# Performance work log

Measured on AMD Instinct MI355X. Metric: run time of the kernel, lower is better.

## Reference

```python
import jax, jax.numpy as jnp
import numpy as np

CHUNK = 32
EPS = 1e-6

def _l2norm(x):
    return x * jax.lax.rsqrt(jnp.sum(x * x, axis=-1, keepdims=True) + EPS)

def setup_inputs() -> dict:
    key = jax.random.key(0)
    k1, k2, k3, k4 = jax.random.split(key, 4)
    b, h, L, dk, dv = 4, 8, 4096, 128, 128
    return {
        'q': jax.random.normal(k1, (b, h, L, dk), dtype=jnp.float32),
        'k': jax.random.normal(k2, (b, h, L, dk), dtype=jnp.float32),
        'v': jax.random.normal(k3, (b, h, L, dv), dtype=jnp.float32),
        'beta': jax.random.uniform(k4, (b, h, L), dtype=jnp.float32),
    }

def _delta_rule_chunkwise(q, k, v, beta):
    b, h, L, dk = q.shape
    dv = v.shape[-1]
    c = CHUNK
    assert L % c == 0, 'L must be a multiple of chunk_size (no padding path)'
    n = L // c

    q = _l2norm(q)
    k = _l2norm(k)
    v = v * beta[..., None]
    k_beta = k * beta[..., None]

    # [b,h,n,c,d]
    resh = lambda t: t.reshape(b, h, n, c, t.shape[-1])
    qc, kc, vc, kbc = resh(q), resh(k), resh(v), resh(k_beta)

    ones = jnp.ones((c, c), dtype=jnp.float32)
    strict_lower = jnp.tril(ones, -1)      # below diagonal
    lower_inc = jnp.tril(ones, 0)          # diagonal and below

    # inv = -(k_beta @ k^T) with upper-incl-diag zeroed, then forward substitution
    inv = -jnp.einsum('bhncd,bhned->bhnce', kbc, kc) * strict_lower
    for i in range(1, c):
        # inv[..., i, :i] += inv[..., i, :] @ inv[..., :, :i]
        upd = jnp.einsum('bhnk,bhnkj->bhnj', inv[..., i, :], inv[..., :, :i])
        inv = inv.at[..., i, :i].add(upd)
    inv = inv + jnp.eye(c, dtype=inv.dtype)

    u = jnp.einsum('bhnce,bhned->bhncd', inv, vc)    # [b,h,n,c,dv]
    w = jnp.einsum('bhnce,bhned->bhncd', inv, kbc)   # [b,h,n,c,dk]

    # scan over chunks carrying state S [b,h,dk,dv]
    def step(S, inp):
        q_i, k_i, u0_i, w_i = inp  # [b,h,c,d*]
        attn = jnp.einsum('bhcd,bhed->bhce', q_i, k_i) * lower_inc
        u_i = u0_i - jnp.einsum('bhcd,bhdv->bhcv', w_i, S)
        out_i = jnp.einsum('bhcd,bhdv->bhcv', q_i, S) + jnp.einsum('bhce,bhev->bhcv', attn, u_i)
        S = S + jnp.einsum('bhcd,bhcv->bhdv', k_i, u_i)
        return S, out_i

    chunk_first = lambda t: jnp.moveaxis(t, 2, 0)  # [n,b,h,c,d]
    S0 = jnp.zeros((b, h, dk, dv), dtype=q.dtype)
    S, out = jax.lax.scan(step, S0, (chunk_first(qc), chunk_first(kc), chunk_first(u), chunk_first(w)))
    out = jnp.moveaxis(out, 0, 2).reshape(b, h, L, dv)
    return out, S

def reference(q, k, v, beta):
    out, S = _delta_rule_chunkwise(q, k, v, beta)
    return out
```

## Files before the change

### kernel.cpp

```cpp
#include <hip/hip_runtime.h>
#include <math.h>

#define CHUNK 32
#define DK 128
#define DV 128
#define L_SEQ 4096
#define BH 32
#define NCH 128

typedef __attribute__((ext_vector_type(8))) short bf16x8;
typedef __attribute__((ext_vector_type(4))) float f32x4;

union U8 { unsigned int u[4]; bf16x8 v; };

#define MFMA16(a, b, c) __builtin_amdgcn_mfma_f32_16x16x32_bf16((a), (b), (c), 0, 0, 0)
#define LGKM_WAIT() __asm__ __volatile__("s_waitcnt lgkmcnt(0)" ::: "memory")

__device__ __forceinline__ unsigned short f2bf(float x){
    unsigned int u = __builtin_bit_cast(unsigned int, x);
    u = u + 0x7FFFu + ((u >> 16) & 1u);
    return (unsigned short)(u >> 16);
}
__device__ __forceinline__ unsigned int pk2(float a, float b){
    unsigned int r;
    asm("v_cvt_pk_bf16_f32 %0, %1, %2" : "=v"(r) : "v"(a), "v"(b));
    return r;
}

__device__ __forceinline__ bf16x8 afragF32(const float (*M)[36], int row, int q8){
    float4 f0 = *(const float4*)&M[row][q8];
    float4 f1 = *(const float4*)&M[row][q8 + 4];
    U8 t;
    t.u[0] = pk2(f0.x, f0.y); t.u[1] = pk2(f0.z, f0.w);
    t.u[2] = pk2(f1.x, f1.y); t.u[3] = pk2(f1.z, f1.w);
    return t.v;
}
__device__ __forceinline__ bf16x8 bfragF32(const float (*M)[36], int q8, int col){
    U8 t;
#pragma unroll
    for (int j2 = 0; j2 < 4; ++j2)
        t.u[j2] = pk2(M[q8 + 2*j2][col], M[q8 + 2*j2 + 1][col]);
    return t.v;
}


template<bool WKT>
__global__ __launch_bounds__(64)
void prep_kernel(const float* __restrict__ q, const float* __restrict__ k,
                 const float* __restrict__ beta,
                 unsigned short* __restrict__ qw, unsigned short* __restrict__ kw,
                 unsigned short* __restrict__ Tw, unsigned short* __restrict__ Aw,
                 unsigned short* __restrict__ kwT)
{
    const int bc = blockIdx.x;
    const size_t row0 = (size_t)bc * CHUNK;
    const int l = threadIdx.x;
    const int quad = (l >> 4) & 3, ln15 = l & 15, q8 = quad * 8;

    __shared__ float Ms[32][36];
    __shared__ float Rs[32][36];
    __shared__ unsigned short knS[WKT ? 4392 : 2];

    const float bet0 = beta[row0 + ln15];
    const float bet1 = beta[row0 + 16 + ln15];

    bf16x8 qF[2][4];
    {
        float4 raw[2][4][2];
        float s0 = 0.f, s1 = 0.f;
#pragma unroll
        for (int mt = 0; mt < 2; ++mt)
#pragma unroll
        for (int ks = 0; ks < 4; ++ks){
            const float* p = q + (row0 + 16*mt + ln15) * DK + 32*ks + q8;
            raw[mt][ks][0] = *(const float4*)p;
            raw[mt][ks][1] = *(const float4*)(p + 4);
        }
#pragma unroll
        for (int ks = 0; ks < 4; ++ks)
#pragma unroll
        for (int h = 0; h < 2; ++h){
            float4 a = raw[0][ks][h], b = raw[1][ks][h];
            s0 += a.x*a.x + a.y*a.y + a.z*a.z + a.w*a.w;
            s1 += b.x*b.x + b.y*b.y + b.z*b.z + b.w*b.w;
        }
        s0 += __shfl_xor(s0, 16); s0 += __shfl_xor(s0, 32);
        s1 += __shfl_xor(s1, 16); s1 += __shfl_xor(s1, 32);
        float sc0 = rsqrtf(s0 + 1e-6f), sc1 = rsqrtf(s1 + 1e-6f);
#pragma unroll
        for (int mt = 0; mt < 2; ++mt){
            float sc = mt ? sc1 : sc0;
#pragma unroll
            for (int ks = 0; ks < 4; ++ks){
                float4 a = raw[mt][ks][0], b = raw[mt][ks][1];
// ... 16 lines not shown
            const float* p = k + (row0 + 16*mt + ln15) * DK + 32*ks + q8;
            raw[mt][ks][0] = *(const float4*)p;
            raw[mt][ks][1] = *(const float4*)(p + 4);
        }
#pragma unroll
        for (int ks = 0; ks < 4; ++ks)
#pragma unroll
        for (int h = 0; h < 2; ++h){
            float4 a = raw[0][ks][h], b = raw[1][ks][h];
            s0 += a.x*a.x + a.y*a.y + a.z*a.z + a.w*a.w;
            s1 += b.x*b.x + b.y*b.y + b.z*b.z + b.w*b.w;
        }
        s0 += __shfl_xor(s0, 16); s0 += __shfl_xor(s0, 32);
        s1 += __shfl_xor(s1, 16); s1 += __shfl_xor(s1, 32);
        float sc0 = rsqrtf(s0 + 1e-6f), sc1 = rsqrtf(s1 + 1e-6f);
#pragma unroll
        for (int mt = 0; mt < 2; ++mt){
            float sc = mt ? sc1 : sc0;
            float bb = mt ? bet1 : bet0;
#pragma unroll
            for (int ks = 0; ks < 4; ++ks){
                float4 a = raw[mt][ks][0], b = raw[mt][ks][1];
                float x0=a.x*sc, x1=a.y*sc, x2=a.z*sc, x3=a.w*sc;
                float x4=b.x*sc, x5=b.y*sc, x6=b.z*sc, x7=b.w*sc;
                U8 t, tb;
                t.u[0]=pk2(x0,x1); t.u[1]=pk2(x2,x3); t.u[2]=pk2(x4,x5); t.u[3]=pk2(x6,x7);
                tb.u[0]=pk2(x0*bb,x1*bb); tb.u[1]=pk2(x2*bb,x3*bb);
                tb.u[2]=pk2(x4*bb,x5*bb); tb.u[3]=pk2(x6*bb,x7*bb);
                kF[mt][ks] = t.v; kB[mt][ks] = tb.v;
                *(bf16x8*)(kw + (row0 + 16*mt + ln15) * DK + 32*ks + q8) = t.v;
            }
        }
    }

    if constexpr (WKT){
#pragma unroll
        for (int mt = 0; mt < 2; ++mt)
#pragma unroll
        for (int ks = 0; ks < 4; ++ks){
            int i = 16*mt + ln15;
            int ad = i * 136 + (i >> 3) * 16 + 32*ks + q8;
            *(bf16x8*)&knS[ad] = kF[mt][ks];
        }
    }

    f32x4 Z = {0.f, 0.f, 0.f, 0.f};
    f32x4 Bacc[2][2] = {{Z, Z}, {Z, Z}};
    f32x4 Aacc[2][2] = {{Z, Z}, {Z, Z}};
#pragma unroll
    for (int ks = 0; ks < 4; ++ks)
#pragma unroll
    for (int mt = 0; mt < 2; ++mt)
#pragma unroll
    for (int nt = 0; nt < 2; ++nt){
        Bacc[mt][nt] = MFMA16(kB[mt][ks], kF[nt][ks], Bacc[mt][nt]);
        Aacc[mt][nt] = MFMA16(qF[mt][ks], kF[nt][ks], Aacc[mt][nt]);
    }

    f32x4 Rc[2][2];
#pragma unroll
    for (int mt = 0; mt < 2; ++mt)
#pragma unroll
    for (int nt = 0; nt < 2; ++nt)
#pragma unroll
    for (int rg = 0; rg < 4; ++rg){
        int row = 16*mt + 4*quad + rg, col = 16*nt + ln15;
        float av = (col <= row) ? Aacc[mt][nt][rg] : 0.f;
        Aw[((size_t)bc << 10) + row*32 + col] = f2bf(av);
        float bm = (col < row) ? -Bacc[mt][nt][rg] : 0.f;
        Ms[row][col] = bm;
        Rc[mt][nt][rg] = bm + ((col == row) ? 1.f : 0.f);
    }

    if constexpr (WKT){
        unsigned short* kT = kwT + ((size_t)bc << 12);
#pragma unroll
        for (int t = 0; t < 8; ++t){
            unsigned short rj[8];
#pragma unroll
            for (int j = 0; j < 8; ++j)
                rj[j] = knS[(q8 + j) * 136 + ((q8 + j) >> 3) * 16 + 16*t + ln15];
            U8 kk;
            kk.u[0] = (unsigned)rj[0] | ((unsigned)rj[1] << 16);
            kk.u[1] = (unsigned)rj[2] | ((unsigned)rj[3] << 16);
            kk.u[2] = (unsigned)rj[4] | ((unsigned)rj[5] << 16);
            kk.u[3] = (unsigned)rj[6] | ((unsigned)rj[7] << 16);
            *(bf16x8*)(kT + (16*t + ln15) * 32 + q8) = kk.v;
        }
    }

#pragma unroll 1
    for (int rd = 0; rd < 4; ++rd){
        LGKM_WAIT();
        bf16x8 Am[2], Bm2[2];
#pragma unroll
        for (int mt = 0; mt < 2; ++mt) Am[mt] = afragF32(Ms, 16*mt + ln15, q8);
#pragma unroll
        for (int nt = 0; nt < 2; ++nt) Bm2[nt] = bfragF32(Ms, q8, 16*nt + ln15);
        f32x4 Mq[2][2];
#pragma unroll
        for (int mt = 0; mt < 2; ++mt)
#pragma unroll
        for (int nt = 0; nt < 2; ++nt)
            Mq[mt][nt] = MFMA16(Am[mt], Bm2[nt], Z);
#pragma unroll
        for (int mt = 0; mt < 2; ++mt)
#pragma unroll
        for (int nt = 0; nt < 2; ++nt)
#pragma unroll
        for (int rg = 0; rg < 4; ++rg){
            int row = 16*mt + 4*quad + rg, col = 16*nt + ln15;
            Rs[row][col] = Rc[mt][nt][rg];
            Ms[row][col] = Mq[mt][nt][rg];
        }
        LGKM_WAIT();
        bf16x8 Ar[2], Bq[2];
#pragma unroll
        for (int mt = 0; mt < 2; ++mt) Ar[mt] = afragF32(Rs, 16*mt + ln15, q8);
#pragma unroll
        for (int nt = 0; nt < 2; ++nt) Bq[nt] = bfragF32(Ms, q8, 16*nt + ln15);
#pragma unroll
        for (int mt = 0; mt < 2; ++mt)
#pragma unroll
        for (int nt = 0; nt < 2; ++nt)
            Rc[mt][nt] = MFMA16(Ar[mt], Bq[nt], Rc[mt][nt]);
    }

#pragma unroll
    for (int mt = 0; mt < 2; ++mt)
#pragma unroll
    for (int nt = 0; nt < 2; ++nt)
#pragma unroll
    for (int rg = 0; rg < 4; ++rg){
        int row = 16*mt + 4*quad + rg, col = 16*nt + ln15;
        Tw[((size_t)bc << 10) + row*32 + col] = f2bf(Rc[mt][nt][rg]);
    }
}


__global__ __launch_bounds__(64, 1)
void scan_fast(const float* __restrict__ v, const float* __restrict__ beta,
               const unsigned short* __restrict__ qw, const unsigned short* __restrict__ kw,
               const unsigned short* __restrict__ kwT,
               const unsigned short* __restrict__ Tw, const unsigned short* __restrict__ Aw,
               float* __restrict__ out)
{
    const int id = blockIdx.x;
    const int bh = id & 31, cb = id >> 5, c0 = cb * 16;
    const int l = threadIdx.x;
    const int quad = (l >> 4) & 3, ln15 = l & 15, q8 = quad * 8;
    const int hi = l >> 5;

    const f32x4 Z = {0.f, 0.f, 0.f, 0.f};
    f32x4 Sacc[8];
#pragma unroll
    for (int t = 0; t < 8; ++t) Sacc[t] = Z;

    const size_t bhL = (size_t)bh * L_SEQ;
    const int a0 = (((l & 16) << 1) | ln15) << 2;
    const int a1 = a0 + 64;

    bf16x8 cur[2][4], qA[2][4], knA[8], tA[2], aA[2], uB;
    float vr[8], br[8];

    auto quadswap = [&](int p0, int p1, int p2, int p3) -> bf16x8 {
        U8 r; int e, f;
        e = __builtin_amdgcn_ds_bpermute(a0, p0); f = __builtin_amdgcn_ds_bpermute(a0, p2);
        r.u[0] = (unsigned)(hi ? f : e);
        e = __builtin_amdgcn_ds_bpermute(a0, p1); f = __builtin_amdgcn_ds_bpermute(a0, p3);
        r.u[1] = (unsigned)(hi ? f : e);
        e = __builtin_amdgcn_ds_bpermute(a1, p0); f = __builtin_amdgcn_ds_bpermute(a1, p2);
// ... 32 lines not shown
            aA[mt] = *(const bf16x8*)(Ap + (16*mt + ln15) * 32 + q8);
    };
    auto loadVB = [&](int ch){
        const size_t row0 = bhL + (size_t)ch * CHUNK;
#pragma unroll
        for (int g = 0; g < 8; ++g){
            int i = 16*(g >> 2) + 4*quad + (g & 3);
            vr[g] = v[(row0 + i) * DV + c0 + ln15];
            br[g] = beta[row0 + i];
        }
    };
    auto loadKT = [&](int ch){
        const unsigned short* p = kwT + ((size_t)(bh * NCH + ch) << 12);
#pragma unroll
        for (int t = 0; t < 8; ++t)
            knA[t] = *(const bf16x8*)(p + (16*t + ln15) * 32 + q8);
    };

    loadK(0); loadQ(0); loadT(0); loadA(0); loadVB(0);
    {
        U8 z; z.u[0] = 0u; z.u[1] = 0u; z.u[2] = 0u; z.u[3] = 0u;
        uB = z.v;
#pragma unroll
        for (int t = 0; t < 8; ++t) knA[t] = z.v;
    }

    for (int ch = 0; ch < NCH; ++ch){
        const size_t row0 = bhL + (size_t)ch * CHUNK;
        const int chn = (ch + 1 < NCH) ? ch + 1 : NCH - 1;

#pragma unroll
        for (int t = 0; t < 8; ++t)
            Sacc[t] = MFMA16(knA[t], uB, Sacc[t]);

        loadKT(ch);

        int P[8][2];
#pragma unroll
        for (int t = 0; t < 8; ++t){
            P[t][0] = (int)pk2(Sacc[t][0], Sacc[t][1]);
            P[t][1] = (int)pk2(Sacc[t][2], Sacc[t][3]);
        }
        bf16x8 SB[4];
#pragma unroll
        for (int ks = 0; ks < 4; ++ks)
            SB[ks] = quadswap(P[2*ks][0], P[2*ks][1], P[2*ks+1][0], P[2*ks+1][1]);

        f32x4 Y[2] = {Z, Z}, Op[2] = {Z, Z};
#pragma unroll
        for (int ks = 0; ks < 4; ++ks)
#pragma unroll
        for (int mt = 0; mt < 2; ++mt){
            Y[mt]  = MFMA16(cur[mt][ks], SB[ks], Y[mt]);
            Op[mt] = MFMA16(qA[mt][ks],  SB[ks], Op[mt]);
        }

        loadK(chn); loadQ(chn);

        int PX0, PX1, PX2, PX3;
        {
            float x00 = br[0]*(vr[0]-Y[0][0]), x01 = br[1]*(vr[1]-Y[0][1]);
            float x02 = br[2]*(vr[2]-Y[0][2]), x03 = br[3]*(vr[3]-Y[0][3]);
            float x10 = br[4]*(vr[4]-Y[1][0]), x11 = br[5]*(vr[5]-Y[1][1]);
            float x12 = br[6]*(vr[6]-Y[1][2]), x13 = br[7]*(vr[7]-Y[1][3]);
            PX0 = (int)pk2(x00, x01); PX1 = (int)pk2(x02, x03);
            PX2 = (int)pk2(x10, x11); PX3 = (int)pk2(x12, x13);
        }
        bf16x8 Xb = quadswap(PX0, PX1, PX2, PX3);

        f32x4 U[2];
#pragma unroll
        for (int mt = 0; mt < 2; ++mt) U[mt] = MFMA16(tA[mt], Xb, Z);

        loadT(chn);

        {
            int PU0 = (int)pk2(U[0][0], U[0][1]), PU1 = (int)pk2(U[0][2], U[0][3]);
            int PU2 = (int)pk2(U[1][0], U[1][1]), PU3 = (int)pk2(U[1][2], U[1][3]);
            uB = quadswap(PU0, PU1, PU2, PU3);
        }

        f32x4 O[2];
#pragma unroll
        for (int mt = 0; mt < 2; ++mt) O[mt] = MFMA16(aA[mt], uB, Op[mt]);
#pragma unroll
        for (int mt = 0; mt < 2; ++mt)
#pragma unroll
        for (int rg = 0; rg < 4; ++rg)
            out[(row0 + 16*mt + 4*quad + rg) * DV + c0 + ln15] = O[mt][rg];

        loadA(chn);
        loadVB(chn);
    }
}


__global__ __launch_bounds__(64, 1)
void scan_kernel(const float* __restrict__ v, const float* __restrict__ beta,
                 const unsigned short* __restrict__ qw, const unsigned short* __restrict__ kw,
                 const unsigned short* __restrict__ Tw, const unsigned short* __restrict__ Aw,
                 float* __restrict__ out)
{
    const int id = blockIdx.x;
    const int bh = id & 31, cb = id >> 5, c0 = cb * 16;
    const int l = threadIdx.x;
    const int quad = (l >> 4) & 3, ln15 = l & 15, q8 = quad * 8;
    const int hi = l >> 5;

    __shared__ unsigned short knR[4392];
    __shared__ unsigned short Xt[16][40];
    __shared__ unsigned short ut[16][40];

    const f32x4 Z = {0.f, 0.f, 0.f, 0.f};
    f32x4 Sacc[8];
#pragma unroll
    for (int t = 0; t < 8; ++t) Sacc[t] = Z;

    const size_t bhL = (size_t)bh * L_SEQ;
    const int a0 = (((l & 16) << 1) | ln15) << 2;
    const int a1 = a0 + 64;

    bf16x8 kAa[2][4], kAb[2][4];
    bf16x8 qA[2][4], tA[2], aA[2], knA[8], uB;
    float vr[8], br[8];

    auto loadK = [&](int ch, bf16x8 (&kA)[2][4]){
        const unsigned short* kp = kw + (bhL + (size_t)ch * CHUNK) * DK;
#pragma unroll
        for (int mt = 0; mt < 2; ++mt)
#pragma unroll
        for (int ks = 0; ks < 4; ++ks)
            kA[mt][ks] = *(const bf16x8*)(kp + (16*mt + ln15) * DK + 32*ks + q8);
    };
    auto loadQ = [&](int ch){
        const unsigned short* qp = qw + (bhL + (size_t)ch * CHUNK) * DK;
#pragma unroll
        for (int mt = 0; mt < 2; ++mt)
#pragma unroll
        for (int ks = 0; ks < 4; ++ks)
            qA[mt][ks] = *(const bf16x8*)(qp + (16*mt + ln15) * DK + 32*ks + q8);
    };
    auto loadT = [&](int ch){
        const unsigned short* Tp = Tw + ((size_t)(bh * NCH + ch) << 10);
#pragma unroll
        for (int mt = 0; mt < 2; ++mt)
            tA[mt] = *(const bf16x8*)(Tp + (16*mt + ln15) * 32 + q8);
    };
    auto loadA = [&](int ch){
        const unsigned short* Ap = Aw + ((size_t)(bh * NCH + ch) << 10);
#pragma unroll
        for (int mt = 0; mt < 2; ++mt)
            aA[mt] = *(const bf16x8*)(Ap + (16*mt + ln15) * 32 + q8);
    };
    auto loadVB = [&](int ch){
        const size_t row0 = bhL + (size_t)ch * CHUNK;
#pragma unroll
        for (int g = 0; g < 8; ++g){
            int i = 16*(g >> 2) + 4*quad + (g & 3);
            vr[g] = v[(row0 + i) * DV + c0 + ln15];
            br[g] = beta[row0 + i];
        }
    };

    loadK(0, kAa);
    loadQ(0); loadT(0); loadA(0); loadVB(0);
    loadK(1, kAb);
    {
        U8 z; z.u[0] = 0u; z.u[1] = 0u; z.u[2] = 0u; z.u[3] = 0u;
        uB = z.v;
#pragma unroll
        for (int t = 0; t < 8; ++t) knA[t] = z.v;
    }

    auto body = [&](int ch, bf16x8 (&cur)[2][4]){
        const size_t row0 = bhL + (size_t)ch * CHUNK;

#pragma unroll
        for (int t = 0; t < 8; ++t)
            Sacc[t] = MFMA16(knA[t], uB, Sacc[t]);

        int P[8][2];
#pragma unroll
        for (int t = 0; t < 8; ++t){
            P[t][0] = (int)pk2(Sacc[t][0], Sacc[t][1]);
            P[t][1] = (int)pk2(Sacc[t][2], Sacc[t][3]);
        }
        bf16x8 SB[4];
#pragma unroll
        for (int ks = 0; ks < 4; ++ks){
            U8 sb;
            int e, f;
            e = __builtin_amdgcn_ds_bpermute(a0, P[2*ks][0]);
            f = __builtin_amdgcn_ds_bpermute(a0, P[2*ks+1][0]);
            sb.u[0] = (unsigned)(hi ? f : e);
            e = __builtin_amdgcn_ds_bpermute(a0, P[2*ks][1]);
            f = __builtin_amdgcn_ds_bpermute(a0, P[2*ks+1][1]);
            sb.u[1] = (unsigned)(hi ? f : e);
            e = __builtin_amdgcn_ds_bpermute(a1, P[2*ks][0]);
            f = __builtin_amdgcn_ds_bpermute(a1, P[2*ks+1][0]);
            sb.u[2] = (unsigned)(hi ? f : e);
            e = __builtin_amdgcn_ds_bpermute(a1, P[2*ks][1]);
            f = __builtin_amdgcn_ds_bpermute(a1, P[2*ks+1][1]);
            sb.u[3] = (unsigned)(hi ? f : e);
            SB[ks] = sb.v;
        }

        f32x4 Y[2] = {Z, Z}, Op[2] = {Z, Z};
#pragma unroll
        for (int ks = 0; ks < 4; ++ks)
#pragma unroll
        for (int mt = 0; mt < 2; ++mt){
            Y[mt]  = MFMA16(cur[mt][ks], SB[ks], Y[mt]);
            Op[mt] = MFMA16(qA[mt][ks],  SB[ks], Op[mt]);
        }

#pragma unroll
        for (int mt = 0; mt < 2; ++mt){
            unsigned int w0 = pk2(br[4*mt+0] * (vr[4*mt+0] - Y[mt][0]),
                                  br[4*mt+1] * (vr[4*mt+1] - Y[mt][1]));
            unsigned int w1 = pk2(br[4*mt+2] * (vr[4*mt+2] - Y[mt][2]),
                                  br[4*mt+3] * (vr[4*mt+3] - Y[mt][3]));
            *(unsigned int*)&Xt[ln15][16*mt + 4*quad]     = w0;
            *(unsigned int*)&Xt[ln15][16*mt + 4*quad + 2] = w1;
        }

#pragma unroll
        for (int mt = 0; mt < 2; ++mt)
#pragma unroll
        for (int ks = 0; ks < 4; ++ks){
            int i = 16*mt + ln15;
            int ad = i * 136 + (i >> 3) * 16 + 32*ks + q8;
            *(bf16x8*)&knR[ad] = cur[mt][ks];
        }

        bf16x8 Xb = *(const bf16x8*)&Xt[ln15][q8];

        unsigned int rja[32];
#pragma unroll
        for (int t = 0; t < 4; ++t)
#pragma unroll
        for (int j = 0; j < 8; ++j)
            rja[8*t + j] = knR[(q8 + j) * 136 + ((q8 + j) >> 3) * 16 + 16*t + ln15];

        f32x4 U[2];
#pragma unroll
        for (int mt = 0; mt < 2; ++mt) U[mt] = MFMA16(tA[mt], Xb, Z);

#pragma unroll
        for (int mt = 0; mt < 2; ++mt){
            *(unsigned int*)&ut[ln15][16*mt + 4*quad]     = pk2(U[mt][0], U[mt][1]);
            *(unsigned int*)&ut[ln15][16*mt + 4*quad + 2] = pk2(U[mt][2], U[mt][3]);
        }

#pragma unroll
        for (int t = 0; t < 4; ++t){
            U8 kk;
            kk.u[0] = rja[8*t+0] | (rja[8*t+1] << 16);
            kk.u[1] = rja[8*t+2] | (rja[8*t+3] << 16);
            kk.u[2] = rja[8*t+4] | (rja[8*t+5] << 16);
            kk.u[3] = rja[8*t+6] | (rja[8*t+7] << 16);
            knA[t] = kk.v;
        }

        uB = *(const bf16x8*)&ut[ln15][q8];

        const int chn = (ch + 1 < NCH) ? ch + 1 : NCH - 1;
        const int ch2 = (ch + 2 < NCH) ? ch + 2 : NCH - 1;
        loadQ(chn); loadT(chn); loadVB(chn);
        loadK(ch2, cur);

        unsigned int rjb[32];
#pragma unroll
        for (int t = 0; t < 4; ++t)
#pragma unroll
        for (int j = 0; j < 8; ++j)
            rjb[8*t + j] = knR[(q8 + j) * 136 + ((q8 + j) >> 3) * 16 + 16*(t + 4) + ln15];

        f32x4 O[2];
#pragma unroll
        for (int mt = 0; mt < 2; ++mt) O[mt] = MFMA16(aA[mt], uB, Op[mt]);
#pragma unroll
        for (int mt = 0; mt < 2; ++mt)
#pragma unroll
        for (int rg = 0; rg < 4; ++rg)
            out[(row0 + 16*mt + 4*quad + rg) * DV + c0 + ln15] = O[mt][rg];

#pragma unroll
        for (int t = 0; t < 4; ++t){
            U8 kk;
            kk.u[0] = rjb[8*t+0] | (rjb[8*t+1] << 16);
            kk.u[1] = rjb[8*t+2] | (rjb[8*t+3] << 16);
            kk.u[2] = rjb[8*t+4] | (rjb[8*t+5] << 16);
            kk.u[3] = rjb[8*t+6] | (rjb[8*t+7] << 16);
            knA[t + 4] = kk.v;
        }
        loadA(chn);
    };

    for (int ch = 0; ch < NCH; ch += 2){
        body(ch,     kAa);
        body(ch + 1, kAb);
    }
}


__global__ __launch_bounds__(512, 1)
void deltanet_fused(const float* __restrict__ q, const float* __restrict__ k,
                    const float* __restrict__ v, const float* __restrict__ beta,
                    float* __restrict__ out)
{
    const int bh = blockIdx.x;
    const int tid = threadIdx.x;
    const int n = L_SEQ / CHUNK;

    __shared__ float S[DK][DV + 1];
    __shared__ float qs[CHUNK][DK + 1];
    __shared__ float ks[CHUNK][DK + 1];
    __shared__ float vs[CHUNK][DV + 1];
    __shared__ float kbs[CHUNK][DK + 1];
    __shared__ float T[CHUNK][CHUNK + 1];
    __shared__ float at[CHUNK][CHUNK + 1];
    __shared__ float bet[CHUNK];

    for (int idx = tid; idx < DK * DV; idx += 512)
        S[idx / DV][idx % DV] = 0.f;
    __syncthreads();

    const size_t base_bh = (size_t)bh * L_SEQ;

    for (int ch = 0; ch < n; ++ch){
        const size_t row0 = base_bh + (size_t)ch * CHUNK;
        for (int idx = tid; idx < CHUNK * DK; idx += 512){
            int r = idx >> 7, c = idx & 127;
            size_t g = (row0 + (size_t)r) * DK + c;
// ... 100 lines not shown
            for (int r = 0; r < 8; ++r)
                out[(row0 + (size_t)(i0 + r)) * DV + c] = acc[r];
        }
        __syncthreads();
        {
            int c = tid & 127;
            int d0 = (tid >> 7) * 32;
            float acc[32];
#pragma unroll
            for (int r = 0; r < 32; ++r) acc[r] = 0.f;
            for (int i = 0; i < CHUNK; ++i){
                float uv = vs[i][c];
#pragma unroll
                for (int r = 0; r < 32; ++r) acc[r] += ks[i][d0 + r] * uv;
            }
#pragma unroll
            for (int r = 0; r < 32; ++r) S[d0 + r][c] += acc[r];
        }
        __syncthreads();
    }
}

extern "C" void kernel_launch(void* const* d_in, const int* in_sizes, int n_in,
                              void* d_out, int out_size, void* d_ws, size_t ws_size,
                              hipStream_t stream) {
    const float* q = (const float*)d_in[0];
    const float* k = (const float*)d_in[1];
    const float* v = (const float*)d_in[2];
    const float* beta = (const float*)d_in[3];
    float* out = (float*)d_out;

    const size_t QK = (size_t)BH * L_SEQ * DK;
    const size_t TA = (size_t)BH * NCH * 1024;
    const size_t need_full = (3 * QK + 2 * TA) * sizeof(unsigned short);
    const size_t need_mid  = (2 * QK + 2 * TA) * sizeof(unsigned short);

    if (ws_size >= need_full){
        unsigned short* qwp = (unsigned short*)d_ws;
        unsigned short* kwp = qwp + QK;
        unsigned short* Twp = kwp + QK;
        unsigned short* Awp = Twp + TA;
        unsigned short* kTp = Awp + TA;
        prep_kernel<true><<<BH * NCH, 64, 0, stream>>>(q, k, beta, qwp, kwp, Twp, Awp, kTp);
        scan_fast<<<BH * 8, 64, 0, stream>>>(v, beta, qwp, kwp, kTp, Twp, Awp, out);
    } else if (ws_size >= need_mid){
        unsigned short* qwp = (unsigned short*)d_ws;
        unsigned short* kwp = qwp + QK;
        unsigned short* Twp = kwp + QK;
        unsigned short* Awp = Twp + TA;
        prep_kernel<false><<<BH * NCH, 64, 0, stream>>>(q, k, beta, qwp, kwp, Twp, Awp, nullptr);
        scan_kernel<<<BH * 8, 64, 0, stream>>>(v, beta, qwp, kwp, Twp, Awp, out);
    } else {
        deltanet_fused<<<BH, 512, 0, stream>>>(q, k, v, beta, out);
    }
}
```

Baseline: 364.9 us.

## Process chunk pairs per scan step using precomputed cross-chunk G/F matrices

Adds a prep kernel that handles two 32-row chunks per block and precomputes cross-chunk products (odd kbeta·even k and odd q·even k) into new G and F workspaces. The new scan kernel advances the state once per 64-row superchunk, so the serial S-dependent MFMA chain and the state conversion and shuffle run half as often. It also replaces the LDS transposes with ds_bpermute quad swaps. The cost is more registers per lane, extra workspace and extra bf16 rounding in the cross-chunk correction terms. The old mid path is dropped in favour of the previous fast path as the fallback.

```diff
diff --git a/kernel.cpp b/kernel.cpp
--- a/kernel.cpp
+++ b/kernel.cpp
@@ -7,6 +7,7 @@
 #define L_SEQ 4096
 #define BH 32
 #define NCH 128
+#define NSC 64
 
 typedef __attribute__((ext_vector_type(8))) short bf16x8;
 typedef __attribute__((ext_vector_type(4))) float f32x4;
@@ -44,7 +45,452 @@
 }
 
 
-template<bool WKT>
+__global__ __launch_bounds__(64)
+void prep64_kernel(const float* __restrict__ q, const float* __restrict__ k,
+                   const float* __restrict__ beta,
+                   unsigned short* __restrict__ qw, unsigned short* __restrict__ kw,
+                   unsigned short* __restrict__ Tw, unsigned short* __restrict__ Aw,
+                   unsigned short* __restrict__ kwT,
+                   unsigned short* __restrict__ Gw, unsigned short* __restrict__ Fw)
+{
+    const int sb = blockIdx.x;
+    const size_t row0 = (size_t)sb * 64;
+    const int bcE = 2*sb, bcO = 2*sb + 1;
+    const int l = threadIdx.x;
+    const int quad = (l >> 4) & 3, ln15 = l & 15, q8 = quad * 8;
+
+    __shared__ float Ms[32][36];
+    __shared__ float Rs[32][36];
+    __shared__ __align__(16) unsigned short knS[4392];
+
+    const f32x4 Z = {0.f, 0.f, 0.f, 0.f};
+
+    auto loadnormQ = [&](size_t r0, bf16x8 (&qF)[2][4]){
+        float4 raw[2][4][2];
+        float s0 = 0.f, s1 = 0.f;
+#pragma unroll
+        for (int mt = 0; mt < 2; ++mt)
+#pragma unroll
+        for (int ks = 0; ks < 4; ++ks){
+            const float* p = q + (r0 + 16*mt + ln15) * DK + 32*ks + q8;
+            raw[mt][ks][0] = *(const float4*)p;
+            raw[mt][ks][1] = *(const float4*)(p + 4);
+        }
+#pragma unroll
+        for (int ks = 0; ks < 4; ++ks)
+#pragma unroll
+        for (int h = 0; h < 2; ++h){
+            float4 a = raw[0][ks][h], b = raw[1][ks][h];
+            s0 += a.x*a.x + a.y*a.y + a.z*a.z + a.w*a.w;
+            s1 += b.x*b.x + b.y*b.y + b.z*b.z + b.w*b.w;
+        }
+        s0 += __shfl_xor(s0, 16); s0 += __shfl_xor(s0, 32);
+        s1 += __shfl_xor(s1, 16); s1 += __shfl_xor(s1, 32);
+        float sc0 = rsqrtf(s0 + 1e-6f), sc1 = rsqrtf(s1 + 1e-6f);
+#pragma unroll
+        for (int mt = 0; mt < 2; ++mt){
+            float sc = mt ? sc1 : sc0;
+#pragma unroll
+            for (int ks = 0; ks < 4; ++ks){
+                float4 a = raw[mt][ks][0], b = raw[mt][ks][1];
+                U8 t;
+                t.u[0] = pk2(a.x*sc, a.y*sc); t.u[1] = pk2(a.z*sc, a.w*sc);
+                t.u[2] = pk2(b.x*sc, b.y*sc); t.u[3] = pk2(b.z*sc, b.w*sc);
+                qF[mt][ks] = t.v;
+                *(bf16x8*)(qw + (r0 + 16*mt + ln15) * DK + 32*ks + q8) = t.v;
+            }
+        }
+    };
+    auto loadnormK = [&](size_t r0, bf16x8 (&kF)[2][4], bf16x8 (&kB)[2][4]){
+        const float b0 = beta[r0 + ln15];
+        const float b1 = beta[r0 + 16 + ln15];
+        float4 raw[2][4][2];
+        float s0 = 0.f, s1 = 0.f;
+#pragma unroll
+        for (int mt = 0; mt < 2; ++mt)
+#pragma unroll
+        for (int ks = 0; ks < 4; ++ks){
+            const float* p = k + (r0 + 16*mt + ln15) * DK + 32*ks + q8;
+            raw[mt][ks][0] = *(const float4*)p;
+            raw[mt][ks][1] = *(const float4*)(p + 4);
+        }
+#pragma unroll
+        for (int ks = 0; ks < 4; ++ks)
+#pragma unroll
+        for (int h = 0; h < 2; ++h){
+            float4 a = raw[0][ks][h], b = raw[1][ks][h];
+            s0 += a.x*a.x + a.y*a.y + a.z*a.z + a.w*a.w;
+            s1 += b.x*b.x + b.y*b.y + b.z*b.z + b.w*b.w;
+        }
+        s0 += __shfl_xor(s0, 16); s0 += __shfl_xor(s0, 32);
+        s1 += __shfl_xor(s1, 16); s1 += __shfl_xor(s1, 32);
+        float sc0 = rsqrtf(s0 + 1e-6f), sc1 = rsqrtf(s1 + 1e-6f);
+#pragma unroll
+        for (int mt = 0; mt < 2; ++mt){
+            float sc = mt ? sc1 : sc0;
+            float bb = mt ? b1 : b0;
+#pragma unroll
+            for (int ks = 0; ks < 4; ++ks){
+                float4 a = raw[mt][ks][0], b = raw[mt][ks][1];
+                float x0=a.x*sc, x1=a.y*sc, x2=a.z*sc, x3=a.w*sc;
+                float x4=b.x*sc, x5=b.y*sc, x6=b.z*sc, x7=b.w*sc;
+                U8 t, tb;
+                t.u[0]=pk2(x0,x1); t.u[1]=pk2(x2,x3); t.u[2]=pk2(x4,x5); t.u[3]=pk2(x6,x7);
+                tb.u[0]=pk2(x0*bb,x1*bb); tb.u[1]=pk2(x2*bb,x3*bb);
+                tb.u[2]=pk2(x4*bb,x5*bb); tb.u[3]=pk2(x6*bb,x7*bb);
+                kF[mt][ks] = t.v; kB[mt][ks] = tb.v;
+                *(bf16x8*)(kw + (r0 + 16*mt + ln15) * DK + 32*ks + q8) = t.v;
+            }
+        }
+    };
+    auto stageKnS = [&](bf16x8 (&kF)[2][4]){
+#pragma unroll
+        for (int mt = 0; mt < 2; ++mt)
+#pragma unroll
+        for (int ks = 0; ks < 4; ++ks){
+            int i = 16*mt + ln15;
+            int ad = i * 136 + (i >> 3) * 16 + 32*ks + q8;
+            *(bf16x8*)&knS[ad] = kF[mt][ks];
+        }
+    };
+    auto gatherKwT = [&](int bc){
+        unsigned short* kT = kwT + ((size_t)bc << 12);
+#pragma unroll
+        for (int t = 0; t < 8; ++t){
+            unsigned short rj[8];
+#pragma unroll
+            for (int j = 0; j < 8; ++j)
+                rj[j] = knS[(q8 + j) * 136 + ((q8 + j) >> 3) * 16 + 16*t + ln15];
+            U8 kk;
+            kk.u[0] = (unsigned)rj[0] | ((unsigned)rj[1] << 16);
+            kk.u[1] = (unsigned)rj[2] | ((unsigned)rj[3] << 16);
+            kk.u[2] = (unsigned)rj[4] | ((unsigned)rj[5] << 16);
+            kk.u[3] = (unsigned)rj[6] | ((unsigned)rj[7] << 16);
+            *(bf16x8*)(kT + (16*t + ln15) * 32 + q8) = kk.v;
+        }
+    };
+    auto invert32 = [&](f32x4 (&Rc)[2][2]){
+#pragma unroll 1
+        for (int rd = 0; rd < 4; ++rd){
+            LGKM_WAIT();
+            bf16x8 Am[2], Bm2[2];
+#pragma unroll
+            for (int mt = 0; mt < 2; ++mt) Am[mt] = afragF32(Ms, 16*mt + ln15, q8);
+#pragma unroll
+            for (int nt = 0; nt < 2; ++nt) Bm2[nt] = bfragF32(Ms, q8, 16*nt + ln15);
+            f32x4 Mq[2][2];
+#pragma unroll
+            for (int mt = 0; mt < 2; ++mt)
+#pragma unroll
+            for (int nt = 0; nt < 2; ++nt)
+                Mq[mt][nt] = MFMA16(Am[mt], Bm2[nt], Z);
+#pragma unroll
+            for (int mt = 0; mt < 2; ++mt)
+#pragma unroll
+            for (int nt = 0; nt < 2; ++nt)
+#pragma unroll
+            for (int rg = 0; rg < 4; ++rg){
+                int row = 16*mt + 4*quad + rg, col = 16*nt + ln15;
+                Rs[row][col] = Rc[mt][nt][rg];
+                Ms[row][col] = Mq[mt][nt][rg];
+            }
+            LGKM_WAIT();
+            bf16x8 Ar[2], Bq[2];
+#pragma unroll
+            for (int mt = 0; mt < 2; ++mt) Ar[mt] = afragF32(Rs, 16*mt + ln15, q8);
+#pragma unroll
+            for (int nt = 0; nt < 2; ++nt) Bq[nt] = bfragF32(Ms, q8, 16*nt + ln15);
+#pragma unroll
+            for (int mt = 0; mt < 2; ++mt)
+#pragma unroll
+            for (int nt = 0; nt < 2; ++nt)
+                Rc[mt][nt] = MFMA16(Ar[mt], Bq[nt], Rc[mt][nt]);
+        }
+    };
+
+    bf16x8 qFe[2][4], kFe[2][4], kBe[2][4];
+    loadnormQ(row0, qFe);
+    loadnormK(row0, kFe, kBe);
+    stageKnS(kFe);
+
+    f32x4 Bacc[2][2] = {{Z,Z},{Z,Z}}, Aacc[2][2] = {{Z,Z},{Z,Z}};
+#pragma unroll
+    for (int ks = 0; ks < 4; ++ks)
+#pragma unroll
+    for (int mt = 0; mt < 2; ++mt)
+#pragma unroll
+    for (int nt = 0; nt < 2; ++nt){
+        Bacc[mt][nt] = MFMA16(kBe[mt][ks], kFe[nt][ks], Bacc[mt][nt]);
+        Aacc[mt][nt] = MFMA16(qFe[mt][ks], kFe[nt][ks], Aacc[mt][nt]);
+    }
+    f32x4 Rc[2][2];
+#pragma unroll
+    for (int mt = 0; mt < 2; ++mt)
+#pragma unroll
+    for (int nt = 0; nt < 2; ++nt)
+#pragma unroll
+    for (int rg = 0; rg < 4; ++rg){
+        int row = 16*mt + 4*quad + rg, col = 16*nt + ln15;
+        float av = (col <= row) ? Aacc[mt][nt][rg] : 0.f;
+        Aw[((size_t)bcE << 10) + row*32 + col] = f2bf(av);
+        float bm = (col < row) ? -Bacc[mt][nt][rg] : 0.f;
+        Ms[row][col] = bm;
+        Rc[mt][nt][rg] = bm + ((col == row) ? 1.f : 0.f);
+    }
+    gatherKwT(bcE);
+    invert32(Rc);
+#pragma unroll
+    for (int mt = 0; mt < 2; ++mt)
+#pragma unroll
+    for (int nt = 0; nt < 2; ++nt)
+#pragma unroll
+    for (int rg = 0; rg < 4; ++rg){
+        int row = 16*mt + 4*quad + rg, col = 16*nt + ln15;
+        Tw[((size_t)bcE << 10) + row*32 + col] = f2bf(Rc[mt][nt][rg]);
+    }
+
+    bf16x8 qFo[2][4], kFo[2][4], kBo[2][4];
+    loadnormQ(row0 + 32, qFo);
+    loadnormK(row0 + 32, kFo, kBo);
+    LGKM_WAIT();
+    stageKnS(kFo);
+
+    f32x4 Gacc[2][2] = {{Z,Z},{Z,Z}}, Facc[2][2] = {{Z,Z},{Z,Z}};
+    f32x4 Bo[2][2]   = {{Z,Z},{Z,Z}}, Ao[2][2]   = {{Z,Z},{Z,Z}};
+#pragma unroll
+    for (int ks = 0; ks < 4; ++ks)
+#pragma unroll
+    for (int mt = 0; mt < 2; ++mt)
+#pragma unroll
+    for (int nt = 0; nt < 2; ++nt){
+        Gacc[mt][nt] = MFMA16(kBo[mt][ks], kFe[nt][ks], Gacc[mt][nt]);
+        Facc[mt][nt] = MFMA16(qFo[mt][ks], kFe[nt][ks], Facc[mt][nt]);
+        Bo[mt][nt]   = MFMA16(kBo[mt][ks], kFo[nt][ks], Bo[mt][nt]);
+        Ao[mt][nt]   = MFMA16(qFo[mt][ks], kFo[nt][ks], Ao[mt][nt]);
+    }
+#pragma unroll
+    for (int mt = 0; mt < 2; ++mt)
+#pragma unroll
+    for (int nt = 0; nt < 2; ++nt)
+#pragma unroll
+    for (int rg = 0; rg < 4; ++rg){
+        int row = 16*mt + 4*quad + rg, col = 16*nt + ln15;
+        Fw[((size_t)sb << 10) + row*32 + col] = f2bf(Facc[mt][nt][rg]);
+        Gw[((size_t)sb << 10) + row*32 + col] = f2bf(Gacc[mt][nt][rg]);
+        float av = (col <= row) ? Ao[mt][nt][rg] : 0.f;
+        Aw[((size_t)bcO << 10) + row*32 + col] = f2bf(av);
+        float bm = (col < row) ? -Bo[mt][nt][rg] : 0.f;
+        Ms[row][col] = bm;
+        Rc[mt][nt][rg] = bm + ((col == row) ? 1.f : 0.f);
+    }
+    gatherKwT(bcO);
+    invert32(Rc);
+#pragma unroll
+    for (int mt = 0; mt < 2; ++mt)
+#pragma unroll
+    for (int nt = 0; nt < 2; ++nt)
+#pragma unroll
+    for (int rg = 0; rg < 4; ++rg){
+        int row = 16*mt + 4*quad + rg, col = 16*nt + ln15;
+        Tw[((size_t)bcO << 10) + row*32 + col] = f2bf(Rc[mt][nt][rg]);
+    }
+}
+
+
+__global__ __launch_bounds__(64, 1)
+void scan64(const float* __restrict__ v, const float* __restrict__ beta,
+            const unsigned short* __restrict__ qw, const unsigned short* __restrict__ kw,
+            const unsigned short* __restrict__ kwT, const unsigned short* __restrict__ Tw,
+            const unsigned short* __restrict__ Aw, const unsigned short* __restrict__ Gw,
+            const unsigned short* __restrict__ Fw, float* __restrict__ out)
+{
+    const int id = blockIdx.x;
+    const int bh = id & 31, cb = id >> 5, c0 = cb * 16;
+    const int l = threadIdx.x;
+    const int quad = (l >> 4) & 3, ln15 = l & 15, q8 = quad * 8;
+    const int hi = l >> 5;
+    const f32x4 Z = {0.f, 0.f, 0.f, 0.f};
+
+    f32x4 Sacc[8];
+#pragma unroll
+    for (int t = 0; t < 8; ++t) Sacc[t] = Z;
+
+    const size_t bhL = (size_t)bh * L_SEQ;
+    const int a0 = (((l & 16) << 1) | ln15) << 2;
+    const int a1 = a0 + 64;
+
+    auto quadswap = [&](int p0, int p1, int p2, int p3) -> bf16x8 {
+        U8 r; int e, f;
+        e = __builtin_amdgcn_ds_bpermute(a0, p0); f = __builtin_amdgcn_ds_bpermute(a0, p2);
+        r.u[0] = (unsigned)(hi ? f : e);
+        e = __builtin_amdgcn_ds_bpermute(a0, p1); f = __builtin_amdgcn_ds_bpermute(a0, p3);
+        r.u[1] = (unsigned)(hi ? f : e);
+        e = __builtin_amdgcn_ds_bpermute(a1, p0); f = __builtin_amdgcn_ds_bpermute(a1, p2);
+        r.u[2] = (unsigned)(hi ? f : e);
+        e = __builtin_amdgcn_ds_bpermute(a1, p1); f = __builtin_amdgcn_ds_bpermute(a1, p3);
+        r.u[3] = (unsigned)(hi ? f : e);
+        return r.v;
+    };
+
+    bf16x8 knF[4][4], qA[4][4], knAe[8], knAo[8];
+    bf16x8 t0A[2], t1A[2], gA[2], aAe[2], aAo[2], fA[2];
+    bf16x8 uBe, uBo;
+    float vr[16], br[16];
+
+    auto loadKF = [&](int sc){
+        const unsigned short* p = kw + (bhL + (size_t)sc * 64) * DK;
+#pragma unroll
+        for (int mt = 0; mt < 4; ++mt)
+#pragma unroll
+        for (int ks = 0; ks < 4; ++ks)
+            knF[mt][ks] = *(const bf16x8*)(p + (16*mt + ln15) * DK + 32*ks + q8);
+    };
+    auto loadQA = [&](int sc){
+        const unsigned short* p = qw + (bhL + (size_t)sc * 64) * DK;
+#pragma unroll
+        for (int mt = 0; mt < 4; ++mt)
+#pragma unroll
+        for (int ks = 0; ks < 4; ++ks)
+            qA[mt][ks] = *(const bf16x8*)(p + (16*mt + ln15) * DK + 32*ks + q8);
+    };
+    auto loadKT = [&](int sc){
+        const unsigned short* p = kwT + ((size_t)(bh * NCH + 2*sc) << 12);
+#pragma unroll
+        for (int t = 0; t < 8; ++t)
+            knAe[t] = *(const bf16x8*)(p + (16*t + ln15) * 32 + q8);
+        p += 4096;
+#pragma unroll
+        for (int t = 0; t < 8; ++t)
+            knAo[t] = *(const bf16x8*)(p + (16*t + ln15) * 32 + q8);
+    };
+    auto loadTLAF = [&](int sc){
+        const unsigned short* pT = Tw + ((size_t)(bh * NCH + 2*sc) << 10);
+        const unsigned short* pA = Aw + ((size_t)(bh * NCH + 2*sc) << 10);
+        const unsigned short* pG = Gw + ((size_t)(bh * NSC + sc) << 10);
+        const unsigned short* pF = Fw + ((size_t)(bh * NSC + sc) << 10);
+#pragma unroll
+        for (int m = 0; m < 2; ++m){
+            int off = (16*m + ln15) * 32 + q8;
+            t0A[m] = *(const bf16x8*)(pT + off);
+            t1A[m] = *(const bf16x8*)(pT + 1024 + off);
+            gA[m]  = *(const bf16x8*)(pG + off);
+            aAe[m] = *(const bf16x8*)(pA + off);
+            aAo[m] = *(const bf16x8*)(pA + 1024 + off);
+            fA[m]  = *(const bf16x8*)(pF + off);
+        }
+    };
+    auto loadVB = [&](int sc){
+        const size_t r0 = bhL + (size_t)sc * 64;
+#pragma unroll
+        for (int mt = 0; mt < 4; ++mt)
+#pragma unroll
+        for (int rg = 0; rg < 4; ++rg){
+            int i = 16*mt + 4*quad + rg;
+            vr[4*mt+rg] = v[(r0 + i) * DV + c0 + ln15];
+            br[4*mt+rg] = beta[r0 + i];
+        }
+    };
+
+    loadKF(0); loadQA(0); loadVB(0);
+    {
+        U8 z; z.u[0]=0u; z.u[1]=0u; z.u[2]=0u; z.u[3]=0u;
+        uBe = z.v; uBo = z.v;
+#pragma unroll
+        for (int t = 0; t < 8; ++t){ knAe[t] = z.v; knAo[t] = z.v; }
+    }
+
+    for (int sc = 0; sc < NSC; ++sc){
+        const size_t r0 = bhL + (size_t)sc * 64;
+        const int scn = (sc + 1 < NSC) ? sc + 1 : NSC - 1;
+
+        loadTLAF(sc);
+
+#pragma unroll
+        for (int t = 0; t < 8; ++t) Sacc[t] = MFMA16(knAe[t], uBe, Sacc[t]);
+#pragma unroll
+        for (int t = 0; t < 8; ++t) Sacc[t] = MFMA16(knAo[t], uBo, Sacc[t]);
+
+        loadKT(sc);
+
+        int P[8][2];
+#pragma unroll
+        for (int t = 0; t < 8; ++t){
+            P[t][0] = (int)pk2(Sacc[t][0], Sacc[t][1]);
+            P[t][1] = (int)pk2(Sacc[t][2], Sacc[t][3]);
+        }
+        bf16x8 SB[4];
+#pragma unroll
+        for (int ks = 0; ks < 4; ++ks)
+            SB[ks] = quadswap(P[2*ks][0], P[2*ks][1], P[2*ks+1][0], P[2*ks+1][1]);
+
+        f32x4 Y[4] = {Z,Z,Z,Z}, Op[4] = {Z,Z,Z,Z};
+#pragma unroll
+        for (int ks = 0; ks < 4; ++ks)
+#pragma unroll
+        for (int mt = 0; mt < 4; ++mt){
+            Y[mt]  = MFMA16(knF[mt][ks], SB[ks], Y[mt]);
+            Op[mt] = MFMA16(qA[mt][ks],  SB[ks], Op[mt]);
+        }
+
+        loadKF(scn); loadQA(scn);
+
+        int PXE[2][2];
+#pragma unroll
+        for (int mt = 0; mt < 2; ++mt){
+            float x0 = br[4*mt+0] * (vr[4*mt+0] - Y[mt][0]);
+            float x1 = br[4*mt+1] * (vr[4*mt+1] - Y[mt][1]);
+            float x2 = br[4*mt+2] * (vr[4*mt+2] - Y[mt][2]);
+            float x3 = br[4*mt+3] * (vr[4*mt+3] - Y[mt][3]);
+            PXE[mt][0] = (int)pk2(x0, x1);
+            PXE[mt][1] = (int)pk2(x2, x3);
+        }
+        bf16x8 Xb0 = quadswap(PXE[0][0], PXE[0][1], PXE[1][0], PXE[1][1]);
+
+        f32x4 U0 = MFMA16(t0A[0], Xb0, Z);
+        f32x4 U1 = MFMA16(t0A[1], Xb0, Z);
+
+        uBe = quadswap((int)pk2(U0[0],U0[1]), (int)pk2(U0[2],U0[3]),
+                       (int)pk2(U1[0],U1[1]), (int)pk2(U1[2],U1[3]));
+
+        f32x4 Gc0 = MFMA16(gA[0], uBe, Z);
+        f32x4 Gc1 = MFMA16(gA[1], uBe, Z);
+        int PXO[2][2];
+        {
+            float x0 = br[8]  * (vr[8]  - Y[2][0]) - Gc0[0];
+            float x1 = br[9]  * (vr[9]  - Y[2][1]) - Gc0[1];
+            float x2 = br[10] * (vr[10] - Y[2][2]) - Gc0[2];
+            float x3 = br[11] * (vr[11] - Y[2][3]) - Gc0[3];
+            PXO[0][0] = (int)pk2(x0, x1); PXO[0][1] = (int)pk2(x2, x3);
+            float y0 = br[12] * (vr[12] - Y[3][0]) - Gc1[0];
+            float y1 = br[13] * (vr[13] - Y[3][1]) - Gc1[1];
+            float y2 = br[14] * (vr[14] - Y[3][2]) - Gc1[2];
+            float y3 = br[15] * (vr[15] - Y[3][3]) - Gc1[3];
+            PXO[1][0] = (int)pk2(y0, y1); PXO[1][1] = (int)pk2(y2, y3);
+        }
+        bf16x8 Xb1 = quadswap(PXO[0][0], PXO[0][1], PXO[1][0], PXO[1][1]);
+
+        loadVB(scn);
+
+        f32x4 U2 = MFMA16(t1A[0], Xb1, Z);
+        f32x4 U3 = MFMA16(t1A[1], Xb1, Z);
+
+        uBo = quadswap((int)pk2(U2[0],U2[1]), (int)pk2(U2[2],U2[3]),
+                       (int)pk2(U3[0],U3[1]), (int)pk2(U3[2],U3[3]));
+
+        f32x4 O[4];
+        O[0] = MFMA16(aAe[0], uBe, Op[0]);
+        O[1] = MFMA16(aAe[1], uBe, Op[1]);
+        O[2] = MFMA16(fA[0], uBe, Op[2]); O[2] = MFMA16(aAo[0], uBo, O[2]);
+        O[3] = MFMA16(fA[1], uBe, Op[3]); O[3] = MFMA16(aAo[1], uBo, O[3]);
+#pragma unroll
+        for (int mt = 0; mt < 4; ++mt)
+#pragma unroll
+        for (int rg = 0; rg < 4; ++rg)
+            out[(r0 + 16*mt + 4*quad + rg) * DV + c0 + ln15] = O[mt][rg];
+    }
+}
+
+
 __global__ __launch_bounds__(64)
 void prep_kernel(const float* __restrict__ q, const float* __restrict__ k,
                  const float* __restrict__ beta,
@@ -59,7 +505,7 @@
 
     __shared__ float Ms[32][36];
     __shared__ float Rs[32][36];
-    __shared__ unsigned short knS[WKT ? 4392 : 2];
+    __shared__ unsigned short knS[4392];
 
     const float bet0 = beta[row0 + ln15];
     const float bet1 = beta[row0 + 16 + ln15];
@@ -142,18 +588,14 @@
             }
         }
     }
-
-    if constexpr (WKT){
-#pragma unroll
-        for (int mt = 0; mt < 2; ++mt)
-#pragma unroll
-        for (int ks = 0; ks < 4; ++ks){
-            int i = 16*mt + ln15;
-            int ad = i * 136 + (i >> 3) * 16 + 32*ks + q8;
-            *(bf16x8*)&knS[ad] = kF[mt][ks];
-        }
-    }
-
+#pragma unroll
+    for (int mt = 0; mt < 2; ++mt)
+#pragma unroll
+    for (int ks = 0; ks < 4; ++ks){
+        int i = 16*mt + ln15;
+        int ad = i * 136 + (i >> 3) * 16 + 32*ks + q8;
+        *(bf16x8*)&knS[ad] = kF[mt][ks];
+    }
     f32x4 Z = {0.f, 0.f, 0.f, 0.f};
     f32x4 Bacc[2][2] = {{Z, Z}, {Z, Z}};
     f32x4 Aacc[2][2] = {{Z, Z}, {Z, Z}};
@@ -166,7 +608,6 @@
         Bacc[mt][nt] = MFMA16(kB[mt][ks], kF[nt][ks], Bacc[mt][nt]);
         Aacc[mt][nt] = MFMA16(qF[mt][ks], kF[nt][ks], Aacc[mt][nt]);
     }
-
     f32x4 Rc[2][2];
 #pragma unroll
     for (int mt = 0; mt < 2; ++mt)
@@ -181,8 +622,7 @@
         Ms[row][col] = bm;
         Rc[mt][nt][rg] = bm + ((col == row) ? 1.f : 0.f);
     }
-
-    if constexpr (WKT){
+    {
         unsigned short* kT = kwT + ((size_t)bc << 12);
 #pragma unroll
         for (int t = 0; t < 8; ++t){
@@ -198,7 +638,6 @@
             *(bf16x8*)(kT + (16*t + ln15) * 32 + q8) = kk.v;
         }
     }
-
 #pragma unroll 1
     for (int rd = 0; rd < 4; ++rd){
         LGKM_WAIT();
@@ -235,7 +674,6 @@
         for (int nt = 0; nt < 2; ++nt)
             Rc[mt][nt] = MFMA16(Ar[mt], Bq[nt], Rc[mt][nt]);
     }
-
 #pragma unroll
     for (int mt = 0; mt < 2; ++mt)
 #pragma unroll
@@ -246,7 +684,6 @@
         Tw[((size_t)bc << 10) + row*32 + col] = f2bf(Rc[mt][nt][rg]);
     }
 }
-
 
 __global__ __launch_bounds__(64, 1)
 void scan_fast(const float* __restrict__ v, const float* __restrict__ beta,
@@ -345,7 +782,6 @@
 #pragma unroll
         for (int t = 0; t < 8; ++t)
             Sacc[t] = MFMA16(knA[t], uB, Sacc[t]);
-
         loadKT(ch);
 
         int P[8][2];
@@ -367,7 +803,6 @@
             Y[mt]  = MFMA16(cur[mt][ks], SB[ks], Y[mt]);
             Op[mt] = MFMA16(qA[mt][ks],  SB[ks], Op[mt]);
         }
-
         loadK(chn); loadQ(chn);
 
         int PX0, PX1, PX2, PX3;
@@ -384,7 +819,6 @@
         f32x4 U[2];
 #pragma unroll
         for (int mt = 0; mt < 2; ++mt) U[mt] = MFMA16(tA[mt], Xb, Z);
-
         loadT(chn);
 
         {
@@ -404,215 +838,6 @@
 
         loadA(chn);
         loadVB(chn);
-    }
-}
-
-
-__global__ __launch_bounds__(64, 1)
-void scan_kernel(const float* __restrict__ v, const float* __restrict__ beta,
-                 const unsigned short* __restrict__ qw, const unsigned short* __restrict__ kw,
-                 const unsigned short* __restrict__ Tw, const unsigned short* __restrict__ Aw,
-                 float* __restrict__ out)
-{
-    const int id = blockIdx.x;
-    const int bh = id & 31, cb = id >> 5, c0 = cb * 16;
-    const int l = threadIdx.x;
-    const int quad = (l >> 4) & 3, ln15 = l & 15, q8 = quad * 8;
-    const int hi = l >> 5;
-
-    __shared__ unsigned short knR[4392];
-    __shared__ unsigned short Xt[16][40];
-    __shared__ unsigned short ut[16][40];
-
-    const f32x4 Z = {0.f, 0.f, 0.f, 0.f};
-    f32x4 Sacc[8];
-#pragma unroll
-    for (int t = 0; t < 8; ++t) Sacc[t] = Z;
-
-    const size_t bhL = (size_t)bh * L_SEQ;
-    const int a0 = (((l & 16) << 1) | ln15) << 2;
-    const int a1 = a0 + 64;
-
-    bf16x8 kAa[2][4], kAb[2][4];
-    bf16x8 qA[2][4], tA[2], aA[2], knA[8], uB;
-    float vr[8], br[8];
-
-    auto loadK = [&](int ch, bf16x8 (&kA)[2][4]){
-        const unsigned short* kp = kw + (bhL + (size_t)ch * CHUNK) * DK;
-#pragma unroll
-        for (int mt = 0; mt < 2; ++mt)
-#pragma unroll
-        for (int ks = 0; ks < 4; ++ks)
-            kA[mt][ks] = *(const bf16x8*)(kp + (16*mt + ln15) * DK + 32*ks + q8);
-    };
-    auto loadQ = [&](int ch){
-        const unsigned short* qp = qw + (bhL + (size_t)ch * CHUNK) * DK;
-#pragma unroll
-        for (int mt = 0; mt < 2; ++mt)
-#pragma unroll
-        for (int ks = 0; ks < 4; ++ks)
-            qA[mt][ks] = *(const bf16x8*)(qp + (16*mt + ln15) * DK + 32*ks + q8);
-    };
-    auto loadT = [&](int ch){
-        const unsigned short* Tp = Tw + ((size_t)(bh * NCH + ch) << 10);
-#pragma unroll
-        for (int mt = 0; mt < 2; ++mt)
-            tA[mt] = *(const bf16x8*)(Tp + (16*mt + ln15) * 32 + q8);
-    };
-    auto loadA = [&](int ch){
-        const unsigned short* Ap = Aw + ((size_t)(bh * NCH + ch) << 10);
-#pragma unroll
-        for (int mt = 0; mt < 2; ++mt)
-            aA[mt] = *(const bf16x8*)(Ap + (16*mt + ln15) * 32 + q8);
-    };
-    auto loadVB = [&](int ch){
-        const size_t row0 = bhL + (size_t)ch * CHUNK;
-#pragma unroll
-        for (int g = 0; g < 8; ++g){
-            int i = 16*(g >> 2) + 4*quad + (g & 3);
-            vr[g] = v[(row0 + i) * DV + c0 + ln15];
-            br[g] = beta[row0 + i];
-        }
-    };
-
-    loadK(0, kAa);
-    loadQ(0); loadT(0); loadA(0); loadVB(0);
-    loadK(1, kAb);
-    {
-        U8 z; z.u[0] = 0u; z.u[1] = 0u; z.u[2] = 0u; z.u[3] = 0u;
-        uB = z.v;
-#pragma unroll
-        for (int t = 0; t < 8; ++t) knA[t] = z.v;
-    }
-
-    auto body = [&](int ch, bf16x8 (&cur)[2][4]){
-        const size_t row0 = bhL + (size_t)ch * CHUNK;
-
-#pragma unroll
-        for (int t = 0; t < 8; ++t)
-            Sacc[t] = MFMA16(knA[t], uB, Sacc[t]);
-
-        int P[8][2];
-#pragma unroll
-        for (int t = 0; t < 8; ++t){
-            P[t][0] = (int)pk2(Sacc[t][0], Sacc[t][1]);
-            P[t][1] = (int)pk2(Sacc[t][2], Sacc[t][3]);
-        }
-        bf16x8 SB[4];
-#pragma unroll
-        for (int ks = 0; ks < 4; ++ks){
-            U8 sb;
-            int e, f;
-            e = __builtin_amdgcn_ds_bpermute(a0, P[2*ks][0]);
-            f = __builtin_amdgcn_ds_bpermute(a0, P[2*ks+1][0]);
-            sb.u[0] = (unsigned)(hi ? f : e);
-            e = __builtin_amdgcn_ds_bpermute(a0, P[2*ks][1]);
-            f = __builtin_amdgcn_ds_bpermute(a0, P[2*ks+1][1]);
-            sb.u[1] = (unsigned)(hi ? f : e);
-            e = __builtin_amdgcn_ds_bpermute(a1, P[2*ks][0]);
-            f = __builtin_amdgcn_ds_bpermute(a1, P[2*ks+1][0]);
-            sb.u[2] = (unsigned)(hi ? f : e);
-            e = __builtin_amdgcn_ds_bpermute(a1, P[2*ks][1]);
-            f = __builtin_amdgcn_ds_bpermute(a1, P[2*ks+1][1]);
-            sb.u[3] = (unsigned)(hi ? f : e);
-            SB[ks] = sb.v;
-        }
-
-        f32x4 Y[2] = {Z, Z}, Op[2] = {Z, Z};
-#pragma unroll
-        for (int ks = 0; ks < 4; ++ks)
-#pragma unroll
-        for (int mt = 0; mt < 2; ++mt){
-            Y[mt]  = MFMA16(cur[mt][ks], SB[ks], Y[mt]);
-            Op[mt] = MFMA16(qA[mt][ks],  SB[ks], Op[mt]);
-        }
-
-#pragma unroll
-        for (int mt = 0; mt < 2; ++mt){
-            unsigned int w0 = pk2(br[4*mt+0] * (vr[4*mt+0] - Y[mt][0]),
-                                  br[4*mt+1] * (vr[4*mt+1] - Y[mt][1]));
-            unsigned int w1 = pk2(br[4*mt+2] * (vr[4*mt+2] - Y[mt][2]),
-                                  br[4*mt+3] * (vr[4*mt+3] - Y[mt][3]));
-            *(unsigned int*)&Xt[ln15][16*mt + 4*quad]     = w0;
-            *(unsigned int*)&Xt[ln15][16*mt + 4*quad + 2] = w1;
-        }
-
-#pragma unroll
-        for (int mt = 0; mt < 2; ++mt)
-#pragma unroll
-        for (int ks = 0; ks < 4; ++ks){
-            int i = 16*mt + ln15;
-            int ad = i * 136 + (i >> 3) * 16 + 32*ks + q8;
-            *(bf16x8*)&knR[ad] = cur[mt][ks];
-        }
-
-        bf16x8 Xb = *(const bf16x8*)&Xt[ln15][q8];
-
-        unsigned int rja[32];
-#pragma unroll
-        for (int t = 0; t < 4; ++t)
-#pragma unroll
-        for (int j = 0; j < 8; ++j)
-            rja[8*t + j] = knR[(q8 + j) * 136 + ((q8 + j) >> 3) * 16 + 16*t + ln15];
-
-        f32x4 U[2];
-#pragma unroll
-        for (int mt = 0; mt < 2; ++mt) U[mt] = MFMA16(tA[mt], Xb, Z);
-
-#pragma unroll
-        for (int mt = 0; mt < 2; ++mt){
-            *(unsigned int*)&ut[ln15][16*mt + 4*quad]     = pk2(U[mt][0], U[mt][1]);
-            *(unsigned int*)&ut[ln15][16*mt + 4*quad + 2] = pk2(U[mt][2], U[mt][3]);
-        }
-
-#pragma unroll
-        for (int t = 0; t < 4; ++t){
-            U8 kk;
-            kk.u[0] = rja[8*t+0] | (rja[8*t+1] << 16);
-            kk.u[1] = rja[8*t+2] | (rja[8*t+3] << 16);
-            kk.u[2] = rja[8*t+4] | (rja[8*t+5] << 16);
-            kk.u[3] = rja[8*t+6] | (rja[8*t+7] << 16);
-            knA[t] = kk.v;
-        }
-
-        uB = *(const bf16x8*)&ut[ln15][q8];
-
-        const int chn = (ch + 1 < NCH) ? ch + 1 : NCH - 1;
-        const int ch2 = (ch + 2 < NCH) ? ch + 2 : NCH - 1;
-        loadQ(chn); loadT(chn); loadVB(chn);
-        loadK(ch2, cur);
-
-        unsigned int rjb[32];
-#pragma unroll
-        for (int t = 0; t < 4; ++t)
-#pragma unroll
-        for (int j = 0; j < 8; ++j)
-            rjb[8*t + j] = knR[(q8 + j) * 136 + ((q8 + j) >> 3) * 16 + 16*(t + 4) + ln15];
-
-        f32x4 O[2];
-#pragma unroll
-        for (int mt = 0; mt < 2; ++mt) O[mt] = MFMA16(aA[mt], uB, Op[mt]);
-#pragma unroll
-        for (int mt = 0; mt < 2; ++mt)
-#pragma unroll
-        for (int rg = 0; rg < 4; ++rg)
-            out[(row0 + 16*mt + 4*quad + rg) * DV + c0 + ln15] = O[mt][rg];
-
-#pragma unroll
-        for (int t = 0; t < 4; ++t){
-            U8 kk;
-            kk.u[0] = rjb[8*t+0] | (rjb[8*t+1] << 16);
-            kk.u[1] = rjb[8*t+2] | (rjb[8*t+3] << 16);
-            kk.u[2] = rjb[8*t+4] | (rjb[8*t+5] << 16);
-            kk.u[3] = rjb[8*t+6] | (rjb[8*t+7] << 16);
-            knA[t + 4] = kk.v;
-        }
-        loadA(chn);
-    };
-
-    for (int ch = 0; ch < NCH; ch += 2){
-        body(ch,     kAa);
-        body(ch + 1, kAb);
     }
 }
 
@@ -779,24 +1004,28 @@
 
     const size_t QK = (size_t)BH * L_SEQ * DK;
     const size_t TA = (size_t)BH * NCH * 1024;
-    const size_t need_full = (3 * QK + 2 * TA) * sizeof(unsigned short);
-    const size_t need_mid  = (2 * QK + 2 * TA) * sizeof(unsigned short);
-
-    if (ws_size >= need_full){
+    const size_t TB = (size_t)BH * NSC * 1024;
+    const size_t need64 = (3*QK + 2*TA + 2*TB) * sizeof(unsigned short);
+    const size_t need32 = (3*QK + 2*TA) * sizeof(unsigned short);
+
+    if (ws_size >= need64){
         unsigned short* qwp = (unsigned short*)d_ws;
         unsigned short* kwp = qwp + QK;
         unsigned short* Twp = kwp + QK;
         unsigned short* Awp = Twp + TA;
         unsigned short* kTp = Awp + TA;
-        prep_kernel<true><<<BH * NCH, 64, 0, stream>>>(q, k, beta, qwp, kwp, Twp, Awp, kTp);
-        scan_fast<<<BH * 8, 64, 0, stream>>>(v, beta, qwp, kwp, kTp, Twp, Awp, out);
-    } else if (ws_size >= need_mid){
+        unsigned short* Gwp = kTp + QK;
+        unsigned short* Fwp = Gwp + TB;
+        prep64_kernel<<<BH * NSC, 64, 0, stream>>>(q, k, beta, qwp, kwp, Twp, Awp, kTp, Gwp, Fwp);
+        scan64<<<BH * 8, 64, 0, stream>>>(v, beta, qwp, kwp, kTp, Twp, Awp, Gwp, Fwp, out);
+    } else if (ws_size >= need32){
         unsigned short* qwp = (unsigned short*)d_ws;
         unsigned short* kwp = qwp + QK;
         unsigned short* Twp = kwp + QK;
         unsigned short* Awp = Twp + TA;
-        prep_kernel<false><<<BH * NCH, 64, 0, stream>>>(q, k, beta, qwp, kwp, Twp, Awp, nullptr);
-        scan_kernel<<<BH * 8, 64, 0, stream>>>(v, beta, qwp, kwp, Twp, Awp, out);
+        unsigned short* kTp = Awp + TA;
+        prep_kernel<<<BH * NCH, 64, 0, stream>>>(q, k, beta, qwp, kwp, Twp, Awp, kTp);
+        scan_fast<<<BH * 8, 64, 0, stream>>>(v, beta, qwp, kwp, kTp, Twp, Awp, out);
     } else {
         deltanet_fused<<<BH, 512, 0, stream>>>(q, k, v, beta, out);
     }
```

Measured after the change: 366.4 us. About the same (+0.4%).
